# Kernel tuning notes

Hardware: AMD Instinct MI355X
Metric: run time of the kernel (lower is better)

The kernel has to match this reference:

```python
import jax, jax.numpy as jnp
import numpy as np

TOD, DOW = 288, 7
INPUT_LEN, OUTPUT_LEN = 12, 12
N_NODES, R_PATCH, LAYERS = 883, 8, 3
D_IN, D_NODE, D_TOD, D_DOW = 64, 32, 32, 32
DIMS = D_IN + D_NODE + D_TOD + D_DOW  # 160
HID = 2 * DIMS
NEG = -1e9  # finite large-negative mask (avoids NaN on fully-masked rows)


def setup_inputs():
    key = jax.random.key(0)
    ks = jax.random.split(key, 16)
    B = 8
    x = jax.random.normal(ks[0], (B, INPUT_LEN, N_NODES, 1), jnp.float32)
    te = jax.random.randint(ks[1], (B, INPUT_LEN, N_NODES, 2), 0, 7, dtype=jnp.int32)
    s = 0.1
    return {
        "x": x,
        "te": te,
        "patch_emb": jax.random.normal(ks[2], (R_PATCH, D_NODE), jnp.float32) * s,
        "node_table": jax.random.normal(ks[3], (N_NODES, D_NODE), jnp.float32) * s,
        "tod_emb": jax.random.normal(ks[4], (TOD, D_TOD), jnp.float32) * s,
        "dow_emb": jax.random.normal(ks[5], (DOW, D_DOW), jnp.float32) * s,
        "conv_W": jax.random.normal(ks[6], (D_IN, 3, INPUT_LEN), jnp.float32) * s,
        "conv_b": jnp.zeros((D_IN,), jnp.float32),
        # 4 layernorms per layer: [iro1, iro2, ier1, ier2]
        "ln_scale": jnp.ones((LAYERS, 4, DIMS), jnp.float32),
        "ln_bias": jnp.zeros((LAYERS, 4, DIMS), jnp.float32),
        # attn: axis1 = [iro, ier]; axis2 = [q, k, v, out], weights stored [in, out]
        "attn_W": jax.random.normal(ks[7], (LAYERS, 2, 4, DIMS, DIMS), jnp.float32) * 0.05,
        "attn_b": jnp.zeros((LAYERS, 2, 4, DIMS), jnp.float32),
        "mlp_W1": jax.random.normal(ks[8], (LAYERS, 2, DIMS, HID), jnp.float32) * 0.05,
        "mlp_b1": jnp.zeros((LAYERS, 2, HID), jnp.float32),
        "mlp_W2": jax.random.normal(ks[9], (LAYERS, 2, HID, DIMS), jnp.float32) * 0.05,
        "mlp_b2": jnp.zeros((LAYERS, 2, DIMS), jnp.float32),
        "out_W": jax.random.normal(ks[10], (OUTPUT_LEN, DIMS), jnp.float32) * 0.05,
        "out_b": jnp.zeros((OUTPUT_LEN,), jnp.float32),
    }


def _layernorm(x, g, b):
    mu = jnp.mean(x, axis=-1, keepdims=True)
    var = jnp.mean(jnp.square(x - mu), axis=-1, keepdims=True)
    return (x - mu) / jnp.sqrt(var + 1e-5) * g + b


def _mha(x, W, b, key_mask):
    # single-head attention (num_heads=1 in PatchID); x: [..., S, D]
    q = x @ W[0] + b[0]
    k = x @ W[1] + b[1]
    v = x @ W[2] + b[2]
    score = jnp.einsum('...sd,...td->...st', q, k) / np.sqrt(x.shape[-1]).astype(np.float32)
    score = jnp.where(key_mask[..., None, :], score, NEG)
    w = jax.nn.softmax(score, axis=-1)
    o = jnp.einsum('...st,...td->...sd', w, v)
    return o @ W[3] + b[3]


def _forward(x, te, patch_emb, node_table, tod_emb, dow_emb, conv_W, conv_b,
             ln_scale, ln_bias, attn_W, attn_b, mlp_W1, mlp_b1, mlp_W2, mlp_b2,
             out_W, out_b):
    N, R = N_NODES, R_PATCH
    # ---- PatchClassifier (router) ----
    logits = node_table @ patch_emb.T                       # [N, R]
    probs = jax.nn.softmax(logits, axis=-1)
    patch_ids = jnp.argmax(probs, axis=-1)                  # [N]
    hard = jax.nn.one_hot(patch_ids, R, dtype=probs.dtype)
    probs_st = hard - jax.lax.stop_gradient(probs) + probs  # straight-through
    node_soft = probs @ patch_emb                           # [N, D_NODE]
    # ---- embedding ----
    B, T_in = x.shape[0], x.shape[1]
    T = T_in // INPUT_LEN  # = 1
    tef = te.astype(x.dtype)
    x1 = jnp.concatenate([x, tef[..., 0:1] / TOD, tef[..., 1:2] / DOW], axis=-1)  # [B,T_in,N,3]
    x1 = x1.reshape(B, T, INPUT_LEN, N, 3)
    feat = jnp.einsum('btlnc,dcl->btnd', x1, conv_W) + conv_b  # patchified conv
    tid = te[:, -T:, :, 0]
    diw = te[:, -T:, :, 1]
    emb = jnp.concatenate([
        feat, tod_emb[tid], dow_emb[diw],
        jnp.broadcast_to(node_soft, (B, T, N, D_NODE)),
    ], axis=-1)                                             # [B,T,N,DIMS]
    # ---- group_by_patch (static P = N upper bound, masked) ----
    onehot = patch_ids[:, None] == jnp.arange(R)[None, :]
    pos = jnp.cumsum(onehot.astype(jnp.int32), axis=0)[jnp.arange(N), patch_ids] - 1
    P = N
    pf = jnp.zeros((B, T, R, P, DIMS), emb.dtype).at[:, :, patch_ids, pos, :].set(emb)
    mask2d = jnp.zeros((R, P), bool).at[patch_ids, pos].set(True)
    km_iro = mask2d[None, None]       # [1,1,R,P] valid-key mask, keys = P axis
    km_ier = mask2d.T[None, None]     # [1,1,P,R] valid-key mask, keys = R axis
    # ---- encoder layers ----
    for l in range(LAYERS):
        # intra-patch attention over P
        xn = _layernorm(pf, ln_scale[l, 0], ln_bias[l, 0])
        pf = pf + _mha(xn, attn_W[l, 0], attn_b[l, 0], km_iro)
        h = _layernorm(pf, ln_scale[l, 1], ln_bias[l, 1])
        pf = pf + (jax.nn.gelu(h @ mlp_W1[l, 0] + mlp_b1[l, 0], approximate=False)
                   @ mlp_W2[l, 0] + mlp_b2[l, 0])
        # inter-patch attention over R
        xt = jnp.swapaxes(pf, 2, 3)  # [B,T,P,R,D]
        xn = _layernorm(xt, ln_scale[l, 2], ln_bias[l, 2])
        xt = xt + _mha(xn, attn_W[l, 1], attn_b[l, 1], km_ier)
        pf = jnp.swapaxes(xt, 2, 3)
        h = _layernorm(pf, ln_scale[l, 3], ln_bias[l, 3])
        pf = pf + (jax.nn.gelu(h @ mlp_W1[l, 1] + mlp_b1[l, 1], approximate=False)
                   @ mlp_W2[l, 1] + mlp_b2[l, 1])
    # ---- ungroup + 1x1 output conv ----
    out_feat = pf[:, :, patch_ids, pos, :]                  # [B,T,N,DIMS]
    pred = jnp.einsum('btnd,od->bont', out_feat, out_W) + out_b[None, :, None, None]
    return pred, probs_st


def reference(x, te, patch_emb, node_table, tod_emb, dow_emb, conv_W, conv_b,
              ln_scale, ln_bias, attn_W, attn_b, mlp_W1, mlp_b1, mlp_W2, mlp_b2,
              out_W, out_b):
    return _forward(x, te, patch_emb, node_table, tod_emb, dow_emb, conv_W, conv_b,
                    ln_scale, ln_bias, attn_W, attn_b, mlp_W1, mlp_b1, mlp_W2,
                    mlp_b2, out_W, out_b)
```

## Files before the change

### kernel.cpp

```cpp
#include <hip/hip_runtime.h>
#include <hip/hip_cooperative_groups.h>
#include <math.h>

namespace cg = cooperative_groups;

#define NNODES 883
#define BB 8
#define DIMS_ 160
#define HID_ 320
#define PBB 1008
#define RMAX2 (BB*PBB)
#define RMAXP (RMAX2+64)
#define GXNUM (RMAX2/16)

typedef __attribute__((ext_vector_type(8))) short short8v;
typedef __attribute__((ext_vector_type(4))) float fx4;
typedef __attribute__((ext_vector_type(4))) unsigned short ushort4v;

__device__ __forceinline__ unsigned short f2bf(float f) {
  unsigned int u = __float_as_uint(f);
  u = (u + 0x7fffu + ((u >> 16) & 1u)) >> 16;
  return (unsigned short)u;
}
__device__ __forceinline__ float bf2f(unsigned short u) {
  return __uint_as_float(((unsigned int)u) << 16);
}
__device__ __forceinline__ float gelu_f(float v) {
  return 0.5f*v*(1.f + erff(v*0.70710678118654752f));
}

__global__ __launch_bounds__(256)
void zero_pf(float4* __restrict__ p, int n4) {
  int i = blockIdx.x*256 + threadIdx.x;
  if (i < n4) p[i] = float4{0.f, 0.f, 0.f, 0.f};
}

__global__ __launch_bounds__(1024)
void patch_scan(const float* __restrict__ node_table,
                const float* __restrict__ patch_emb,
                float* __restrict__ probs_st,
                float* __restrict__ nsoft,
                int* __restrict__ pk, int* __restrict__ cnt,
                int* __restrict__ offs) {
  __shared__ float pe[256];
  __shared__ int pid_s[NNODES];
  __shared__ int cnt_s[8], offs_s[8];
  int t = threadIdx.x;
  for (int k = t; k < 256; k += 1024) pe[k] = patch_emb[k];
  if (t < 8) cnt_s[t] = 0;
  __syncthreads();
  int am = -1;
  if (t < NNODES) {
    float nt[32];
#pragma unroll
    for (int j = 0; j < 32; ++j) nt[j] = node_table[t*32 + j];
    float lg[8];
#pragma unroll
    for (int r = 0; r < 8; ++r) {
      float a = 0.f;
#pragma unroll
      for (int j = 0; j < 32; ++j) a += nt[j] * pe[r*32 + j];
      lg[r] = a;
    }
    float m = lg[0];
#pragma unroll
    for (int r = 1; r < 8; ++r) m = fmaxf(m, lg[r]);
    float e[8]; float s = 0.f;
#pragma unroll
    for (int r = 0; r < 8; ++r) { e[r] = expf(lg[r] - m); s += e[r]; }
    float p[8];
#pragma unroll
    for (int r = 0; r < 8; ++r) p[r] = e[r] / s;
    am = 0; float best = p[0];
#pragma unroll
    for (int r = 1; r < 8; ++r) if (p[r] > best) { best = p[r]; am = r; }
    pid_s[t] = am;
    atomicAdd(&cnt_s[am], 1);
#pragma unroll
    for (int r = 0; r < 8; ++r) {
      float hard = (r == am) ? 1.f : 0.f;
      probs_st[t*8 + r] = (hard - p[r]) + p[r];
    }
#pragma unroll
    for (int j = 0; j < 32; ++j) {
      float a = 0.f;
#pragma unroll
      for (int r = 0; r < 8; ++r) a += p[r] * pe[r*32 + j];
      nsoft[t*32 + j] = a;
    }
  }
  __syncthreads();
  if (t == 0) {
    int o = 0;
#pragma unroll
    for (int r = 0; r < 8; ++r) {
      offs_s[r] = o; offs[r] = o; cnt[r] = cnt_s[r];
      o += (cnt_s[r] + 15) & ~15;
    }
  }
  __syncthreads();
  if (t < NNODES) {
    int pos = 0;
    for (int m = 0; m < t; ++m) pos += (pid_s[m] == am) ? 1 : 0;
    pk[t] = offs_s[am] + pos;
  }
}

__global__ __launch_bounds__(160)
void embed_kernel(const float* __restrict__ x, const int* __restrict__ te,
                  const float* __restrict__ convW, const float* __restrict__ convB,
                  const float* __restrict__ tod, const float* __restrict__ dow,
                  const float* __restrict__ nsoft, const int* __restrict__ pk,
                  const float* __restrict__ g, const float* __restrict__ bt,
                  float* __restrict__ pf, unsigned short* __restrict__ xn) {
  int n = blockIdx.x, b = blockIdx.y, t = threadIdx.x;
  __shared__ float xs[3][12];
  __shared__ float rsum[160], rss[160];
  __shared__ float musv[2];
  if (t < 12) {
    int l = t;
    xs[0][l] = x[(b*12 + l)*NNODES + n];
    int base = ((b*12 + l)*NNODES + n)*2;
    xs[1][l] = (float)te[base]     / 288.0f;
    xs[2][l] = (float)te[base + 1] / 7.0f;
  }
  __syncthreads();
  int row = b*PBB + pk[n];
  float val;
  if (t < 64) {
    float a = convB[t];
#pragma unroll
    for (int c = 0; c < 3; ++c)
#pragma unroll
      for (int l = 0; l < 12; ++l)
        a += xs[c][l] * convW[t*36 + c*12 + l];
    val = a;
  } else if (t < 96) {
    int ti = te[((b*12 + 11)*NNODES + n)*2 + 0];
    val = tod[ti*32 + (t - 64)];
  } else if (t < 128) {
    int dw = te[((b*12 + 11)*NNODES + n)*2 + 1];
    val = dow[dw*32 + (t - 96)];
  } else {
    val = nsoft[n*32 + (t - 128)];
  }
  pf[row*DIMS_ + t] = val;
  rsum[t] = val; rss[t] = val*val;
  __syncthreads();
  if (t < 32) {
    float s = 0.f, ss = 0.f;
#pragma unroll
    for (int j = 0; j < 5; ++j) { s += rsum[t + 32*j]; ss += rss[t + 32*j]; }
    s  += __shfl_xor(s, 1, 32);  ss += __shfl_xor(ss, 1, 32);
    s  += __shfl_xor(s, 2, 32);  ss += __shfl_xor(ss, 2, 32);
    s  += __shfl_xor(s, 4, 32);  ss += __shfl_xor(ss, 4, 32);
    s  += __shfl_xor(s, 8, 32);  ss += __shfl_xor(ss, 8, 32);
    s  += __shfl_xor(s, 16, 32); ss += __shfl_xor(ss, 16, 32);
    if (t == 0) {
      float mu = s*(1.f/160.f);
      float var = ss*(1.f/160.f) - mu*mu;
      musv[0] = mu; musv[1] = rsqrtf(var + 1e-5f);
    }
  }
  __syncthreads();
  xn[(size_t)row*DIMS_ + t] = f2bf((val - musv[0])*musv[1]*g[t] + bt[t]);
}

__global__ __launch_bounds__(256)
void cvt_all(const float* __restrict__ attn_W, const float* __restrict__ mlp_W1,
             const float* __restrict__ mlp_W2,
             unsigned short* __restrict__ wt_attn, unsigned short* __restrict__ wt_w1,
             unsigned short* __restrict__ wt_w2) {
  int y = blockIdx.y;
  const float* src; unsigned short* dst; int K, N;
  if (y < 24)      { src = attn_W + (size_t)y*25600;        dst = wt_attn + (size_t)y*25600; K = 160; N = 160; }
  else if (y < 30) { int q = y-24; src = mlp_W1 + (size_t)q*160*320; dst = wt_w1 + (size_t)q*51200; K = 160; N = 320; }
  else             { int q = y-30; src = mlp_W2 + (size_t)q*320*160; dst = wt_w2 + (size_t)q*51200; K = 320; N = 160; }
  int tn = N >> 5, tk = K >> 5;
  int tile = blockIdx.x;
  if (tile >= tn*tk) return;
  int n0 = (tile % tn) << 5, k0 = (tile / tn) << 5;
  __shared__ unsigned short lds[32][33];
  int col = threadIdx.x & 31, rb = threadIdx.x >> 5;
#pragma unroll
  for (int rr = 0; rr < 4; ++rr) {
    int row = rb + 8*rr;
    lds[row][col] = f2bf(src[(size_t)(k0 + row)*N + n0 + col]);
  }
  __syncthreads();
#pragma unroll
  for (int rr = 0; rr < 4; ++rr) {
    int row = rb + 8*rr;
    dst[(size_t)(n0 + row)*K + k0 + col] = lds[col][row];
  }
}

__device__ __forceinline__ void qkv_from_L1(const char* L1,
    const unsigned short* __restrict__ wq, const float* __restrict__ bq,
    unsigned short* __restrict__ qbN, bool transv,
    int row0, int wid, int r15, int kg) {
  constexpr size_t CY = (size_t)(RMAX2 + 16) * DIMS_;
  fx4 accq[4];
#pragma unroll
  for (int u = 0; u < 4; ++u) accq[u] = (fx4){0.f,0.f,0.f,0.f};
#pragma unroll
  for (int t = 0; t < 5; ++t) {
    short8v a4 = *(const short8v*)(const void*)(L1 + r15*384 + ((t*64 + kg*16) ^ ((r15 & 7) << 4)));
#pragma unroll
    for (int u = 0; u < 4; ++u) {
      int n = wid + 8*u;
      if (n < 30) {
        int z = n / 10, nn = n - z*10;
        short8v bfr = *(const short8v*)(const void*)
            (wq + (size_t)z*25600 + (size_t)(nn*16 + r15)*160 + t*32 + kg*8);
        accq[u] = __builtin_amdgcn_mfma_f32_16x16x32_bf16(a4, bfr, accq[u], 0, 0, 0);
      }
    }
  }
#pragma unroll
  for (int u = 0; u < 4; ++u) {
    int n = wid + 8*u;
    if (n >= 30) continue;
    int z = n / 10, nn = n - z*10;
    int col = nn*16 + r15;
    float bv = bq[z*160 + col];
    unsigned short* C = qbN + (size_t)z * CY;
#pragma unroll
    for (int i = 0; i < 4; ++i) {
      int rr = row0 + 4*kg + i;
      unsigned short h = f2bf(accq[u][i] + bv);
      if (transv && z == 2) C[(size_t)col*RMAXP + rr] = h;
      else                  C[(size_t)rr*DIMS_ + col] = h;
    }
  }
}

__global__ __launch_bounds__(512, 4)
void layers_coop(unsigned short* __restrict__ qbA, unsigned short* __restrict__ qbB,
                 const unsigned short* __restrict__ wt_attn,
                 const unsigned short* __restrict__ wt_w1,
                 const unsigned short* __restrict__ wt_w2,
                 const float* __restrict__ attn_b, const float* __restrict__ mlp_b1,
                 const float* __restrict__ mlp_b2,
                 const float* __restrict__ ln_scale, const float* __restrict__ ln_bias,
                 const unsigned short* __restrict__ xn, float* __restrict__ pf,
                 const int* __restrict__ cnt, const int* __restrict__ offs) {
  constexpr size_t CY = (size_t)(RMAX2 + 16) * DIMS_;
  cg::grid_group gg = cg::this_grid();
  __shared__ unsigned short L1s[16*192];
  __shared__ unsigned short L2s[16*320];
  __shared__ float sA[8][16], ssA[8][16];
  __shared__ float Sf[16*256];
  __shared__ unsigned short Pl[16*256];
  __shared__ float Sinv[16];
  __shared__ int cs[8], os[8];
  char* L1 = (char*)L1s; char* L2 = (char*)L2s; char* Pb = (char*)Pl;
  const float scale = 0.07905694150420949f;

  int tid = threadIdx.x;
  int wid = tid >> 6;
  int lane = tid & 63;
  int r15 = lane & 15, kg = lane >> 4;
  int row0 = blockIdx.x * 16;
  if (tid < 8) { cs[tid] = cnt[tid]; os[tid] = offs[tid]; }
  __syncthreads();
  int b = row0 / PBB;
  int local = row0 - b*PBB;
  int r = 7;
#pragma unroll
  for (int rr = 6; rr >= 0; --rr) if (local < os[rr+1]) r = rr;
  int L = cs[r];
  int q0 = local - os[r];
  int bo = b*PBB + os[r];
  int ntP = (wid < 2) ? 2 : 1;
  int ntM = (wid < 4) ? 3 : 2;

  float trunk[2][4];
#pragma unroll
  for (int u = 0; u < 2; ++u)
    if (u < ntP) {
      int col = (wid + 8*u)*16 + r15;
#pragma unroll
      for (int i = 0; i < 4; ++i)
        trunk[u][i] = pf[(size_t)(row0 + 4*kg + i)*DIMS_ + col];
    }

  for (int k = tid; k < 16*DIMS_; k += 512) {
    int row = k / DIMS_, col = k - row*DIMS_;
    int byte = row*384 + ((col*2) ^ ((row & 7) << 4));
    *(unsigned short*)(L1 + byte) = xn[(size_t)(row0 + row)*DIMS_ + col];
  }
  __syncthreads();
  qkv_from_L1(L1, wt_attn, attn_b, qbA, true, row0, wid, r15, kg);
  __threadfence();
  gg.sync();

  for (int wb = 0; wb < 6; ++wb) {
    bool intra = ((wb & 1) == 0);
    bool hasnext = (wb < 5);
    unsigned short* qbCur = (wb & 1) ? qbB : qbA;
    unsigned short* qbNext = (wb & 1) ? qbA : qbB;
    const unsigned short* qb = qbCur;
    const unsigned short* kb = qbCur + CY;
    const unsigned short* vt = qbCur + 2*CY;
    const unsigned short* wqkv = wt_attn + (size_t)wb*4*25600;
    const float* bbase = attn_b + (size_t)wb*4*DIMS_;
    const unsigned short* wproj = wqkv + 3*25600;
    const float* bproj = bbase + 3*DIMS_;
    const unsigned short* w1 = wt_w1 + (size_t)wb*51200;
    const unsigned short* w2 = wt_w2 + (size_t)wb*51200;
    const float* b1v = mlp_b1 + (size_t)wb*HID_;
    const float* b2v = mlp_b2 + (size_t)wb*DIMS_;
    const float* g1  = ln_scale + (size_t)(2*wb + 1)*DIMS_;
    const float* bt1 = ln_bias  + (size_t)(2*wb + 1)*DIMS_;
    const float* gn  = ln_scale + (size_t)(2*wb + 2)*DIMS_;
    const float* btn = ln_bias  + (size_t)(2*wb + 2)*DIMS_;
    const unsigned short* wqkvN = wt_attn + (size_t)(wb+1)*4*25600;
    const float* bqkvN = attn_b + (size_t)(wb+1)*4*DIMS_;

    if (intra) {
      int nkt = (L + 15) >> 4;
      int npv = (L + 31) >> 5;
      short8v qf[5];
      {
        const unsigned short* Qr = qb + (size_t)(row0 + r15)*DIMS_ + kg*8;
#pragma unroll
        for (int kk = 0; kk < 5; ++kk) qf[kk] = *(const short8v*)(const void*)(Qr + kk*32);
      }
#pragma unroll
      for (int u = 0; u < 2; ++u) {
        int t = wid + 8*u;
        if (t < nkt) {
          fx4 a = (fx4){0.f,0.f,0.f,0.f};
          const unsigned short* Kr = kb + (size_t)(bo + t*16 + r15)*DIMS_ + kg*8;
#pragma unroll
          for (int kk = 0; kk < 5; ++kk) {
            short8v kf = *(const short8v*)(const void*)(Kr + kk*32);
            a = __builtin_amdgcn_mfma_f32_16x16x32_bf16(qf[kk], kf, a, 0, 0, 0);
          }
          int j = t*16 + r15;
#pragma unroll
          for (int i = 0; i < 4; ++i)
            Sf[(4*kg + i)*256 + j] = (j < L) ? a[i]*scale : -1e30f;
        }
      }
      __syncthreads();
      {
        int qq = lane >> 5, l32 = lane & 31;
        int row = 2*wid + qq;
        float vals[8];
        float mx = -1e30f;
#pragma unroll
        for (int k = 0; k < 8; ++k) {
          int j = l32 + 32*k;
          float v = (j < L) ? Sf[row*256 + j] : -1e30f;
          vals[k] = v; mx = fmaxf(mx, v);
        }
        mx = fmaxf(mx, __shfl_xor(mx, 1, 32));
        mx = fmaxf(mx, __shfl_xor(mx, 2, 32));
        mx = fmaxf(mx, __shfl_xor(mx, 4, 32));
        mx = fmaxf(mx, __shfl_xor(mx, 8, 32));
        mx = fmaxf(mx, __shfl_xor(mx, 16, 32));
        float sum = 0.f;
#pragma unroll
        for (int k = 0; k < 8; ++k) {
          float e = (vals[k] > -1e29f) ? expf(vals[k] - mx) : 0.f;
          vals[k] = e; sum += e;
        }
        sum += __shfl_xor(sum, 1, 32);
        sum += __shfl_xor(sum, 2, 32);
        sum += __shfl_xor(sum, 4, 32);
        sum += __shfl_xor(sum, 8, 32);
        sum += __shfl_xor(sum, 16, 32);
        if (l32 == 0) Sinv[row] = (sum > 0.f) ? 1.f/sum : 0.f;
#pragma unroll
        for (int k = 0; k < 8; ++k) {
          int j = l32 + 32*k;
          int byte = row*512 + ((j*2) ^ ((row & 7) << 4));
          *(unsigned short*)(Pb + byte) = f2bf(vals[k]);
        }
      }
      __syncthreads();
      fx4 o[2];
#pragma unroll
      for (int u = 0; u < 2; ++u) o[u] = (fx4){0.f,0.f,0.f,0.f};
#pragma unroll
      for (int sS = 0; sS < 8; ++sS) {
        if (sS < npv) {
          short8v pfr = *(const short8v*)(const void*)
              (Pb + r15*512 + ((sS*64 + kg*16) ^ ((r15 & 7) << 4)));
#pragma unroll
          for (int u = 0; u < 2; ++u)
            if (u < ntP) {
              int n = wid + 8*u;
              const unsigned short* Vr = vt + (size_t)(n*16 + r15)*RMAXP + bo + sS*32 + kg*8;
              short8v vf = *(const short8v*)(const void*)Vr;
              o[u] = __builtin_amdgcn_mfma_f32_16x16x32_bf16(pfr, vf, o[u], 0, 0, 0);
            }
        }
      }
      float inv[4];
#pragma unroll
      for (int i = 0; i < 4; ++i) inv[i] = Sinv[4*kg + i];
#pragma unroll
      for (int u = 0; u < 2; ++u)
        if (u < ntP) {
          int n = wid + 8*u;
#pragma unroll
          for (int i = 0; i < 4; ++i) {
            int row = 4*kg + i, d = n*16 + r15;
            int byte = row*384 + ((d*2) ^ ((row & 7) << 4));
            *(unsigned short*)(L1 + byte) = f2bf(o[u][i]*inv[i]);
          }
        }
    } else {
      int qq = lane >> 5, l32 = lane & 31;
      int rowT = 2*wid + qq;
      int p = q0 + rowT;
      bool vq = p < L;
      int j = l32 >> 2, c = l32 & 3;
      int cj = cs[j];
      bool vk = p < cj;
      int keyrow = b*PBB + os[j] + (vk ? p : 0);
      int qrow = row0 + rowT;
      float part = 0.f;
      {
        const unsigned short* qr = qb + (size_t)qrow*DIMS_ + c*40;
        const unsigned short* kr = kb + (size_t)keyrow*DIMS_ + c*40;
#pragma unroll
        for (int dd = 0; dd < 5; ++dd) {
          short8v a8 = *(const short8v*)(const void*)(qr + dd*8);
          short8v b8 = *(const short8v*)(const void*)(kr + dd*8);
#pragma unroll
          for (int u = 0; u < 8; ++u)
            part += bf2f((unsigned short)a8[u]) * bf2f((unsigned short)b8[u]);
        }
      }
      part += __shfl_xor(part, 1, 4);
      part += __shfl_xor(part, 2, 4);
      float sc = (vq && vk) ? part*scale : -1e30f;
      float m = sc;
      m = fmaxf(m, __shfl_xor(m, 4, 32));
      m = fmaxf(m, __shfl_xor(m, 8, 32));
      m = fmaxf(m, __shfl_xor(m, 16, 32));
      float e = (vq && vk) ? expf(sc - m) : 0.f;
      float sum = e;
      sum += __shfl_xor(sum, 4, 32);
      sum += __shfl_xor(sum, 8, 32);
      sum += __shfl_xor(sum, 16, 32);
      float w = (vq && vk && sum > 0.f) ? e/sum : 0.f;
      float o[5];
#pragma unroll
      for (int k = 0; k < 5; ++k) o[k] = 0.f;
      int qbase = qq*32;
#pragma unroll
      for (int jj = 0; jj < 8; ++jj) {
        float wv = __shfl(w, qbase + jj*4);
        int kr2 = __shfl(keyrow, qbase + jj*4);
        if (wv > 0.f) {
          const unsigned short* Vr = vt + (size_t)kr2*DIMS_;
#pragma unroll
          for (int k = 0; k < 5; ++k) o[k] += wv * bf2f(Vr[l32 + 32*k]);
        }
      }
#pragma unroll
      for (int k = 0; k < 5; ++k) {
        int d = l32 + 32*k;
        int byte = rowT*384 + ((d*2) ^ ((rowT & 7) << 4));
        *(unsigned short*)(L1 + byte) = f2bf(vq ? o[k] : 0.f);
      }
    }
    __syncthreads();

    short8v af[5];
#pragma unroll
    for (int t = 0; t < 5; ++t)
      af[t] = *(const short8v*)(const void*)(L1 + r15*384 + ((t*64 + kg*16) ^ ((r15 & 7) << 4)));
    fx4 acc[2];
#pragma unroll
    for (int u = 0; u < 2; ++u) acc[u] = (fx4){0.f,0.f,0.f,0.f};
#pragma unroll
    for (int t = 0; t < 5; ++t)
#pragma unroll
      for (int u = 0; u < 2; ++u)
        if (u < ntP) {
          int n = wid + 8*u;
          short8v bfr = *(const short8v*)(const void*)(wproj + (size_t)(n*16 + r15)*160 + t*32 + kg*8);
          acc[u] = __builtin_amdgcn_mfma_f32_16x16x32_bf16(af[t], bfr, acc[u], 0, 0, 0);
        }

    float sv[4] = {0,0,0,0}, ssv[4] = {0,0,0,0};
#pragma unroll
    for (int u = 0; u < 2; ++u)
      if (u < ntP) {
        int n = wid + 8*u;
        int col = n*16 + r15;
        float bv = bproj[col];
#pragma unroll
        for (int i = 0; i < 4; ++i) {
          float v = trunk[u][i] + acc[u][i] + bv;
          trunk[u][i] = v;
          sv[i] += v; ssv[i] += v*v;
        }
      }
#pragma unroll
    for (int i = 0; i < 4; ++i) {
      sv[i] += __shfl_xor(sv[i], 1, 16); ssv[i] += __shfl_xor(ssv[i], 1, 16);
      sv[i] += __shfl_xor(sv[i], 2, 16); ssv[i] += __shfl_xor(ssv[i], 2, 16);
      sv[i] += __shfl_xor(sv[i], 4, 16); ssv[i] += __shfl_xor(ssv[i], 4, 16);
      sv[i] += __shfl_xor(sv[i], 8, 16); ssv[i] += __shfl_xor(ssv[i], 8, 16);
    }
    if (r15 == 0) {
#pragma unroll
      for (int i = 0; i < 4; ++i) { sA[wid][4*kg+i] = sv[i]; ssA[wid][4*kg+i] = ssv[i]; }
    }
    __syncthreads();
    float mu[4], rs[4];
#pragma unroll
    for (int i = 0; i < 4; ++i) {
      float st = 0.f, sst = 0.f;
#pragma unroll
      for (int w = 0; w < 8; ++w) { st += sA[w][4*kg+i]; sst += ssA[w][4*kg+i]; }
      mu[i] = st*(1.f/160.f);
      float var = sst*(1.f/160.f) - mu[i]*mu[i];
      rs[i] = rsqrtf(var + 1e-5f);
    }
#pragma unroll
    for (int u = 0; u < 2; ++u)
      if (u < ntP) {
        int n = wid + 8*u;
        int col = n*16 + r15;
        float gv = g1[col], bv = bt1[col];
#pragma unroll
        for (int i = 0; i < 4; ++i) {
          int row = 4*kg + i;
          int byte = row*384 + ((col*2) ^ ((row & 7) << 4));
          *(unsigned short*)(L1 + byte) = f2bf((trunk[u][i] - mu[i])*rs[i]*gv + bv);
        }
      }
    __syncthreads();

    fx4 acc2[3];
#pragma unroll
    for (int u = 0; u < 3; ++u) acc2[u] = (fx4){0.f,0.f,0.f,0.f};
#pragma unroll
    for (int t = 0; t < 5; ++t) {
      short8v a2 = *(const short8v*)(const void*)(L1 + r15*384 + ((t*64 + kg*16) ^ ((r15 & 7) << 4)));
#pragma unroll
      for (int u = 0; u < 3; ++u)
        if (u < ntM) {
          int n = wid + 8*u;
          short8v bfr = *(const short8v*)(const void*)(w1 + (size_t)(n*16 + r15)*160 + t*32 + kg*8);
          acc2[u] = __builtin_amdgcn_mfma_f32_16x16x32_bf16(a2, bfr, acc2[u], 0, 0, 0);
        }
    }
#pragma unroll
    for (int u = 0; u < 3; ++u)
      if (u < ntM) {
        int n = wid + 8*u;
        int col = n*16 + r15;
        float bv = b1v[col];
#pragma unroll
        for (int i = 0; i < 4; ++i) {
          float v = gelu_f(acc2[u][i] + bv);
          int row = 4*kg + i;
          int byte = row*640 + ((col*2) ^ ((row & 7) << 4));
          *(unsigned short*)(L2 + byte) = f2bf(v);
        }
      }
    __syncthreads();

    fx4 acc3[2];
#pragma unroll
    for (int u = 0; u < 2; ++u) acc3[u] = (fx4){0.f,0.f,0.f,0.f};
#pragma unroll
    for (int t = 0; t < 10; ++t) {
      short8v a3 = *(const short8v*)(const void*)(L2 + r15*640 + ((t*64 + kg*16) ^ ((r15 & 7) << 4)));
#pragma unroll
      for (int u = 0; u < 2; ++u)
        if (u < ntP) {
          int n = wid + 8*u;
          short8v bfr = *(const short8v*)(const void*)(w2 + (size_t)(n*16 + r15)*320 + t*32 + kg*8);
          acc3[u] = __builtin_amdgcn_mfma_f32_16x16x32_bf16(a3, bfr, acc3[u], 0, 0, 0);
        }
    }
    float sv2[4] = {0,0,0,0}, ssv2[4] = {0,0,0,0};
#pragma unroll
    for (int u = 0; u < 2; ++u)
      if (u < ntP) {
        int n = wid + 8*u;
        int col = n*16 + r15;
        float bv = b2v[col];
#pragma unroll
        for (int i = 0; i < 4; ++i) {
          float v = trunk[u][i] + acc3[u][i] + bv;
          trunk[u][i] = v;
          sv2[i] += v; ssv2[i] += v*v;
        }
      }

    if (hasnext) {
#pragma unroll
      for (int i = 0; i < 4; ++i) {
        sv2[i] += __shfl_xor(sv2[i], 1, 16); ssv2[i] += __shfl_xor(ssv2[i], 1, 16);
        sv2[i] += __shfl_xor(sv2[i], 2, 16); ssv2[i] += __shfl_xor(ssv2[i], 2, 16);
        sv2[i] += __shfl_xor(sv2[i], 4, 16); ssv2[i] += __shfl_xor(ssv2[i], 4, 16);
        sv2[i] += __shfl_xor(sv2[i], 8, 16); ssv2[i] += __shfl_xor(ssv2[i], 8, 16);
      }
      __syncthreads();
      if (r15 == 0) {
#pragma unroll
        for (int i = 0; i < 4; ++i) { sA[wid][4*kg+i] = sv2[i]; ssA[wid][4*kg+i] = ssv2[i]; }
      }
      __syncthreads();
#pragma unroll
      for (int i = 0; i < 4; ++i) {
        float st = 0.f, sst = 0.f;
#pragma unroll
        for (int w = 0; w < 8; ++w) { st += sA[w][4*kg+i]; sst += ssA[w][4*kg+i]; }
        mu[i] = st*(1.f/160.f);
        float var = sst*(1.f/160.f) - mu[i]*mu[i];
        rs[i] = rsqrtf(var + 1e-5f);
      }
#pragma unroll
      for (int u = 0; u < 2; ++u)
        if (u < ntP) {
          int n = wid + 8*u;
          int col = n*16 + r15;
          float gv = gn[col], bv = btn[col];
#pragma unroll
          for (int i = 0; i < 4; ++i) {
            int row = 4*kg + i;
            int byte = row*384 + ((col*2) ^ ((row & 7) << 4));
            *(unsigned short*)(L1 + byte) = f2bf((trunk[u][i] - mu[i])*rs[i]*gv + bv);
          }
        }
      __syncthreads();

      qkv_from_L1(L1, wqkvN, bqkvN, qbNext, (wb & 1) != 0, row0, wid, r15, kg);
      __threadfence();
      gg.sync();
    }
  }

#pragma unroll
  for (int u = 0; u < 2; ++u)
    if (u < ntP) {
      int col = (wid + 8*u)*16 + r15;
#pragma unroll
      for (int i = 0; i < 4; ++i)
        pf[(size_t)(row0 + 4*kg + i)*DIMS_ + col] = trunk[u][i];
    }
}

template<bool INTRA, bool HASNEXT, bool TRANSV_NEXT>
__global__ __launch_bounds__(512)
void fused_layer(const unsigned short* __restrict__ qb,
                 const unsigned short* __restrict__ kb,
                 const unsigned short* __restrict__ vt,
                 const unsigned short* __restrict__ wproj, const float* __restrict__ bproj,
                 const unsigned short* __restrict__ w1, const float* __restrict__ b1v,
                 const unsigned short* __restrict__ w2, const float* __restrict__ b2v,
                 const float* __restrict__ g1, const float* __restrict__ bt1,
                 const float* __restrict__ gn, const float* __restrict__ btn,
                 const unsigned short* __restrict__ wqkvN, const float* __restrict__ bqkvN,
                 float* __restrict__ pf, unsigned short* __restrict__ qbN,
                 const int* __restrict__ cnt, const int* __restrict__ offs) {
  __shared__ unsigned short L1s[16*192];
  __shared__ unsigned short L2s[16*320];
  __shared__ float sA[8][16], ssA[8][16];
  __shared__ float Sf[INTRA ? 16*256 : 1];
  __shared__ unsigned short Pl[INTRA ? 16*256 : 1];
  __shared__ float Sinv[16];
  __shared__ int cs[8], os[8];
  char* L1 = (char*)L1s; char* L2 = (char*)L2s; char* Pb = (char*)Pl;
  const float scale = 0.07905694150420949f;

  int tid = threadIdx.x;
  int wid = tid >> 6;
  int lane = tid & 63;
  int r15 = lane & 15, kg = lane >> 4;
  int row0 = blockIdx.x * 16;
  if (tid < 8) { cs[tid] = cnt[tid]; os[tid] = offs[tid]; }
  __syncthreads();
  int b = row0 / PBB;
  int local = row0 - b*PBB;
  int r = 7;
#pragma unroll
  for (int rr = 6; rr >= 0; --rr) if (local < os[rr+1]) r = rr;
  int L = cs[r];
  int q0 = local - os[r];
  int bo = b*PBB + os[r];
  int ntP = (wid < 2) ? 2 : 1;
  int ntM = (wid < 4) ? 3 : 2;

  if (INTRA) {
    int nkt = (L + 15) >> 4;
    int npv = (L + 31) >> 5;
    short8v qf[5];
    {
      const unsigned short* Qr = qb + (size_t)(row0 + r15)*DIMS_ + kg*8;
#pragma unroll
      for (int kk = 0; kk < 5; ++kk) qf[kk] = *(const short8v*)(const void*)(Qr + kk*32);
    }
#pragma unroll
    for (int u = 0; u < 2; ++u) {
      int t = wid + 8*u;
      if (t < nkt) {
        fx4 a = (fx4){0.f,0.f,0.f,0.f};
        const unsigned short* Kr = kb + (size_t)(bo + t*16 + r15)*DIMS_ + kg*8;
#pragma unroll
        for (int kk = 0; kk < 5; ++kk) {
          short8v kf = *(const short8v*)(const void*)(Kr + kk*32);
          a = __builtin_amdgcn_mfma_f32_16x16x32_bf16(qf[kk], kf, a, 0, 0, 0);
        }
        int j = t*16 + r15;
#pragma unroll
        for (int i = 0; i < 4; ++i)
          Sf[(4*kg + i)*256 + j] = (j < L) ? a[i]*scale : -1e30f;
      }
    }
    __syncthreads();
    {
      int qq = lane >> 5, l32 = lane & 31;
      int row = 2*wid + qq;
      float vals[8];
      float mx = -1e30f;
#pragma unroll
      for (int k = 0; k < 8; ++k) {
        int j = l32 + 32*k;
        float v = (j < L) ? Sf[row*256 + j] : -1e30f;
        vals[k] = v; mx = fmaxf(mx, v);
      }
      mx = fmaxf(mx, __shfl_xor(mx, 1, 32));
      mx = fmaxf(mx, __shfl_xor(mx, 2, 32));
      mx = fmaxf(mx, __shfl_xor(mx, 4, 32));
      mx = fmaxf(mx, __shfl_xor(mx, 8, 32));
      mx = fmaxf(mx, __shfl_xor(mx, 16, 32));
      float sum = 0.f;
#pragma unroll
      for (int k = 0; k < 8; ++k) {
        float e = (vals[k] > -1e29f) ? expf(vals[k] - mx) : 0.f;
        vals[k] = e; sum += e;
      }
      sum += __shfl_xor(sum, 1, 32);
      sum += __shfl_xor(sum, 2, 32);
      sum += __shfl_xor(sum, 4, 32);
      sum += __shfl_xor(sum, 8, 32);
      sum += __shfl_xor(sum, 16, 32);
      if (l32 == 0) Sinv[row] = (sum > 0.f) ? 1.f/sum : 0.f;
#pragma unroll
      for (int k = 0; k < 8; ++k) {
        int j = l32 + 32*k;
        int byte = row*512 + ((j*2) ^ ((row & 7) << 4));
        *(unsigned short*)(Pb + byte) = f2bf(vals[k]);
      }
    }
    __syncthreads();
    fx4 o[2];
#pragma unroll
    for (int u = 0; u < 2; ++u) o[u] = (fx4){0.f,0.f,0.f,0.f};
#pragma unroll
    for (int sS = 0; sS < 8; ++sS) {
      if (sS < npv) {
        short8v pfr = *(const short8v*)(const void*)
            (Pb + r15*512 + ((sS*64 + kg*16) ^ ((r15 & 7) << 4)));
#pragma unroll
        for (int u = 0; u < 2; ++u)
          if (u < ntP) {
            int n = wid + 8*u;
            const unsigned short* Vr = vt + (size_t)(n*16 + r15)*RMAXP + bo + sS*32 + kg*8;
            short8v vf = *(const short8v*)(const void*)Vr;
            o[u] = __builtin_amdgcn_mfma_f32_16x16x32_bf16(pfr, vf, o[u], 0, 0, 0);
          }
      }
    }
    float inv[4];
#pragma unroll
    for (int i = 0; i < 4; ++i) inv[i] = Sinv[4*kg + i];
#pragma unroll
    for (int u = 0; u < 2; ++u)
      if (u < ntP) {
        int n = wid + 8*u;
#pragma unroll
        for (int i = 0; i < 4; ++i) {
          int row = 4*kg + i, d = n*16 + r15;
          int byte = row*384 + ((d*2) ^ ((row & 7) << 4));
          *(unsigned short*)(L1 + byte) = f2bf(o[u][i]*inv[i]);
        }
      }
  } else {
    int qq = lane >> 5, l32 = lane & 31;
    int rowT = 2*wid + qq;
    int p = q0 + rowT;
    bool vq = p < L;
    int j = l32 >> 2, c = l32 & 3;
    int cj = cs[j];
    bool vk = p < cj;
    int keyrow = b*PBB + os[j] + (vk ? p : 0);
    int qrow = row0 + rowT;
    float part = 0.f;
    {
      const unsigned short* qr = qb + (size_t)qrow*DIMS_ + c*40;
      const unsigned short* kr = kb + (size_t)keyrow*DIMS_ + c*40;
#pragma unroll
      for (int dd = 0; dd < 5; ++dd) {
        short8v a8 = *(const short8v*)(const void*)(qr + dd*8);
        short8v b8 = *(const short8v*)(const void*)(kr + dd*8);
#pragma unroll
        for (int u = 0; u < 8; ++u)
          part += bf2f((unsigned short)a8[u]) * bf2f((unsigned short)b8[u]);
      }
    }
    part += __shfl_xor(part, 1, 4);
    part += __shfl_xor(part, 2, 4);
    float sc = (vq && vk) ? part*scale : -1e30f;
    float m = sc;
    m = fmaxf(m, __shfl_xor(m, 4, 32));
    m = fmaxf(m, __shfl_xor(m, 8, 32));
    m = fmaxf(m, __shfl_xor(m, 16, 32));
    float e = (vq && vk) ? expf(sc - m) : 0.f;
    float sum = e;
    sum += __shfl_xor(sum, 4, 32);
    sum += __shfl_xor(sum, 8, 32);
    sum += __shfl_xor(sum, 16, 32);
    float w = (vq && vk && sum > 0.f) ? e/sum : 0.f;
    float o[5];
#pragma unroll
    for (int k = 0; k < 5; ++k) o[k] = 0.f;
    int qbase = qq*32;
#pragma unroll
    for (int jj = 0; jj < 8; ++jj) {
      float wv = __shfl(w, qbase + jj*4);
      int kr2 = __shfl(keyrow, qbase + jj*4);
      if (wv > 0.f) {
        const unsigned short* Vr = vt + (size_t)kr2*DIMS_;
#pragma unroll
        for (int k = 0; k < 5; ++k) o[k] += wv * bf2f(Vr[l32 + 32*k]);
      }
    }
#pragma unroll
    for (int k = 0; k < 5; ++k) {
      int d = l32 + 32*k;
      int byte = rowT*384 + ((d*2) ^ ((rowT & 7) << 4));
      *(unsigned short*)(L1 + byte) = f2bf(vq ? o[k] : 0.f);
    }
  }
  __syncthreads();

  short8v af[5];
#pragma unroll
  for (int t = 0; t < 5; ++t)
    af[t] = *(const short8v*)(const void*)(L1 + r15*384 + ((t*64 + kg*16) ^ ((r15 & 7) << 4)));
  fx4 acc[2];
#pragma unroll
  for (int u = 0; u < 2; ++u) acc[u] = (fx4){0.f,0.f,0.f,0.f};
#pragma unroll
  for (int t = 0; t < 5; ++t)
#pragma unroll
    for (int u = 0; u < 2; ++u)
      if (u < ntP) {
        int n = wid + 8*u;
        short8v bfr = *(const short8v*)(const void*)(wproj + (size_t)(n*16 + r15)*160 + t*32 + kg*8);
        acc[u] = __builtin_amdgcn_mfma_f32_16x16x32_bf16(af[t], bfr, acc[u], 0, 0, 0);
      }

  float pn[2][4];
  float sv[4] = {0,0,0,0}, ssv[4] = {0,0,0,0};
#pragma unroll
  for (int u = 0; u < 2; ++u)
    if (u < ntP) {
      int n = wid + 8*u;
      int col = n*16 + r15;
      float bv = bproj[col];
#pragma unroll
      for (int i = 0; i < 4; ++i) {
        int row = row0 + 4*kg + i;
        float v = pf[(size_t)row*DIMS_ + col] + acc[u][i] + bv;
        pn[u][i] = v;
        pf[(size_t)row*DIMS_ + col] = v;
        sv[i] += v; ssv[i] += v*v;
      }
    }
#pragma unroll
  for (int i = 0; i < 4; ++i) {
    sv[i] += __shfl_xor(sv[i], 1, 16); ssv[i] += __shfl_xor(ssv[i], 1, 16);
    sv[i] += __shfl_xor(sv[i], 2, 16); ssv[i] += __shfl_xor(ssv[i], 2, 16);
    sv[i] += __shfl_xor(sv[i], 4, 16); ssv[i] += __shfl_xor(ssv[i], 4, 16);
    sv[i] += __shfl_xor(sv[i], 8, 16); ssv[i] += __shfl_xor(ssv[i], 8, 16);
  }
  if (r15 == 0) {
#pragma unroll
    for (int i = 0; i < 4; ++i) { sA[wid][4*kg+i] = sv[i]; ssA[wid][4*kg+i] = ssv[i]; }
  }
  __syncthreads();
  float mu[4], rs[4];
#pragma unroll
  for (int i = 0; i < 4; ++i) {
    float st = 0.f, sst = 0.f;
#pragma unroll
    for (int w = 0; w < 8; ++w) { st += sA[w][4*kg+i]; sst += ssA[w][4*kg+i]; }
    mu[i] = st*(1.f/160.f);
    float var = sst*(1.f/160.f) - mu[i]*mu[i];
    rs[i] = rsqrtf(var + 1e-5f);
  }
#pragma unroll
  for (int u = 0; u < 2; ++u)
    if (u < ntP) {
      int n = wid + 8*u;
      int col = n*16 + r15;
      float gv = g1[col], bv = bt1[col];
#pragma unroll
      for (int i = 0; i < 4; ++i) {
        int row = 4*kg + i;
        int byte = row*384 + ((col*2) ^ ((row & 7) << 4));
        *(unsigned short*)(L1 + byte) = f2bf((pn[u][i] - mu[i])*rs[i]*gv + bv);
      }
    }
  __syncthreads();

  fx4 acc2[3];
#pragma unroll
  for (int u = 0; u < 3; ++u) acc2[u] = (fx4){0.f,0.f,0.f,0.f};
#pragma unroll
  for (int t = 0; t < 5; ++t) {
    short8v a2 = *(const short8v*)(const void*)(L1 + r15*384 + ((t*64 + kg*16) ^ ((r15 & 7) << 4)));
#pragma unroll
    for (int u = 0; u < 3; ++u)
      if (u < ntM) {
        int n = wid + 8*u;
        short8v bfr = *(const short8v*)(const void*)(w1 + (size_t)(n*16 + r15)*160 + t*32 + kg*8);
        acc2[u] = __builtin_amdgcn_mfma_f32_16x16x32_bf16(a2, bfr, acc2[u], 0, 0, 0);
      }
  }
#pragma unroll
  for (int u = 0; u < 3; ++u)
    if (u < ntM) {
      int n = wid + 8*u;
      int col = n*16 + r15;
      float bv = b1v[col];
#pragma unroll
      for (int i = 0; i < 4; ++i) {
        float v = gelu_f(acc2[u][i] + bv);
        int row = 4*kg + i;
        int byte = row*640 + ((col*2) ^ ((row & 7) << 4));
        *(unsigned short*)(L2 + byte) = f2bf(v);
      }
    }
  __syncthreads();

  fx4 acc3[2];
#pragma unroll
  for (int u = 0; u < 2; ++u) acc3[u] = (fx4){0.f,0.f,0.f,0.f};
#pragma unroll
  for (int t = 0; t < 10; ++t) {
    short8v a3 = *(const short8v*)(const void*)(L2 + r15*640 + ((t*64 + kg*16) ^ ((r15 & 7) << 4)));
#pragma unroll
    for (int u = 0; u < 2; ++u)
      if (u < ntP) {
        int n = wid + 8*u;
        short8v bfr = *(const short8v*)(const void*)(w2 + (size_t)(n*16 + r15)*320 + t*32 + kg*8);
        acc3[u] = __builtin_amdgcn_mfma_f32_16x16x32_bf16(a3, bfr, acc3[u], 0, 0, 0);
      }
  }
  float sv2[4] = {0,0,0,0}, ssv2[4] = {0,0,0,0};
  float fnv[2][4];
#pragma unroll
  for (int u = 0; u < 2; ++u)
    if (u < ntP) {
      int n = wid + 8*u;
      int col = n*16 + r15;
      float bv = b2v[col];
#pragma unroll
      for (int i = 0; i < 4; ++i) {
        float v = pn[u][i] + acc3[u][i] + bv;
        fnv[u][i] = v;
        pf[(size_t)(row0 + 4*kg + i)*DIMS_ + col] = v;
        sv2[i] += v; ssv2[i] += v*v;
      }
    }
  if (!HASNEXT) return;

#pragma unroll
  for (int i = 0; i < 4; ++i) {
    sv2[i] += __shfl_xor(sv2[i], 1, 16); ssv2[i] += __shfl_xor(ssv2[i], 1, 16);
    sv2[i] += __shfl_xor(sv2[i], 2, 16); ssv2[i] += __shfl_xor(ssv2[i], 2, 16);
    sv2[i] += __shfl_xor(sv2[i], 4, 16); ssv2[i] += __shfl_xor(ssv2[i], 4, 16);
    sv2[i] += __shfl_xor(sv2[i], 8, 16); ssv2[i] += __shfl_xor(ssv2[i], 8, 16);
  }
  __syncthreads();
  if (r15 == 0) {
#pragma unroll
    for (int i = 0; i < 4; ++i) { sA[wid][4*kg+i] = sv2[i]; ssA[wid][4*kg+i] = ssv2[i]; }
  }
  __syncthreads();
#pragma unroll
  for (int i = 0; i < 4; ++i) {
    float st = 0.f, sst = 0.f;
#pragma unroll
    for (int w = 0; w < 8; ++w) { st += sA[w][4*kg+i]; sst += ssA[w][4*kg+i]; }
    mu[i] = st*(1.f/160.f);
    float var = sst*(1.f/160.f) - mu[i]*mu[i];
    rs[i] = rsqrtf(var + 1e-5f);
  }
#pragma unroll
  for (int u = 0; u < 2; ++u)
    if (u < ntP) {
      int n = wid + 8*u;
      int col = n*16 + r15;
      float gv = gn[col], bv = btn[col];
#pragma unroll
      for (int i = 0; i < 4; ++i) {
        int row = 4*kg + i;
        int byte = row*384 + ((col*2) ^ ((row & 7) << 4));
        *(unsigned short*)(L1 + byte) = f2bf((fnv[u][i] - mu[i])*rs[i]*gv + bv);
      }
    }
  __syncthreads();

  qkv_from_L1(L1, wqkvN, bqkvN, qbN, TRANSV_NEXT, row0, wid, r15, kg);
}

__global__ __launch_bounds__(512)
void qkv0_kernel(const unsigned short* __restrict__ xn,
                 const unsigned short* __restrict__ wt_attn, const float* __restrict__ attn_b,
                 unsigned short* __restrict__ qbA) {
  __shared__ unsigned short L1s[16*192];
  char* L1 = (char*)L1s;
  int tid = threadIdx.x;
  int wid = tid >> 6, lane = tid & 63;
  int r15 = lane & 15, kg = lane >> 4;
  int row0 = blockIdx.x * 16;
  for (int k = tid; k < 16*DIMS_; k += 512) {
    int row = k / DIMS_, col = k - row*DIMS_;
    int byte = row*384 + ((col*2) ^ ((row & 7) << 4));
    *(unsigned short*)(L1 + byte) = xn[(size_t)(row0 + row)*DIMS_ + col];
  }
  __syncthreads();
  qkv_from_L1(L1, wt_attn, attn_b, qbA, true, row0, wid, r15, kg);
}

__global__ __launch_bounds__(256)
void out_kernel(const float* __restrict__ pf, const float* __restrict__ outW,
                const float* __restrict__ outB, const int* __restrict__ pk,
                float* __restrict__ out) {
  int idx = blockIdx.x*256 + threadIdx.x;
  if (idx >= BB*12*NNODES) return;
  int n = idx % NNODES;
  int rest = idx / NNODES;
  int o = rest % 12;
  int b = rest / 12;
  int row = b*PBB + pk[n];
  const float4* Pr = (const float4*)&pf[(size_t)row*DIMS_];
  const float4* Wr = (const float4*)&outW[o*DIMS_];
  float ax=0.f, ay=0.f, az=0.f, aw=0.f;
#pragma unroll
  for (int d4 = 0; d4 < 40; ++d4) {
    float4 a = Pr[d4], c = Wr[d4];
    ax += a.x*c.x; ay += a.y*c.y; az += a.z*c.z; aw += a.w*c.w;
  }
  out[idx] = (ax+ay+az+aw) + outB[o];
}

extern "C" void kernel_launch(void* const* d_in, const int* in_sizes, int n_in,
                              void* d_out, int out_size, void* d_ws, size_t ws_size,
                              hipStream_t stream) {
  const float* x         = (const float*)d_in[0];
  const int*   te        = (const int*)d_in[1];
  const float* patch_emb = (const float*)d_in[2];
  const float* node_tab  = (const float*)d_in[3];
  const float* tod_emb   = (const float*)d_in[4];
  const float* dow_emb   = (const float*)d_in[5];
  const float* conv_W    = (const float*)d_in[6];
  const float* conv_b    = (const float*)d_in[7];
  const float* ln_scale  = (const float*)d_in[8];
  const float* ln_bias   = (const float*)d_in[9];
  const float* attn_W    = (const float*)d_in[10];
  const float* attn_b    = (const float*)d_in[11];
  const float* mlp_W1    = (const float*)d_in[12];
  const float* mlp_b1    = (const float*)d_in[13];
  const float* mlp_W2    = (const float*)d_in[14];
  const float* mlp_b2    = (const float*)d_in[15];
  const float* out_W     = (const float*)d_in[16];
  const float* out_b     = (const float*)d_in[17];

  float* out = (float*)d_out;
  float* probs_st = out + BB*12*NNODES;

  const size_t CY = (size_t)(RMAX2 + 16) * DIMS_;
  const size_t QBSZ = 2*CY + (size_t)DIMS_*RMAXP;

  char* W = (char*)d_ws;
  float* pf = (float*)W;                        W += (size_t)(RMAX2 + 16)*DIMS_*4;
  unsigned short* xn = (unsigned short*)W;      W += (size_t)(RMAX2 + 16)*DIMS_*2;
  unsigned short* qbA = (unsigned short*)W;     W += QBSZ*2;
  unsigned short* qbB = (unsigned short*)W;     W += QBSZ*2;
  unsigned short* wt_attn = (unsigned short*)W; W += (size_t)24*160*160*2;
  unsigned short* wt_w1   = (unsigned short*)W; W += (size_t)6*320*160*2;
  unsigned short* wt_w2   = (unsigned short*)W; W += (size_t)6*160*320*2;
  float* nsoft = (float*)W;                     W += (size_t)NNODES*32*4;
  int* pk   = (int*)W;
  int* cnt  = pk + NNODES;
  int* offs = cnt + 8;

  {
    int n4 = (RMAX2 + 16) * DIMS_ / 4;
    zero_pf<<<(n4 + 255)/256, 256, 0, stream>>>((float4*)pf, n4);
  }
  cvt_all<<<dim3(50, 36), 256, 0, stream>>>(attn_W, mlp_W1, mlp_W2, wt_attn, wt_w1, wt_w2);
  patch_scan<<<1, 1024, 0, stream>>>(node_tab, patch_emb, probs_st, nsoft, pk, cnt, offs);
  embed_kernel<<<dim3(NNODES, BB), 160, 0, stream>>>(x, te, conv_W, conv_b, tod_emb, dow_emb,
                                                     nsoft, pk, ln_scale, ln_bias, pf, xn);

  int maxb = 0;
  hipError_t occ = hipOccupancyMaxActiveBlocksPerMultiprocessor(&maxb, (const void*)layers_coop, 512, 0);
  bool coop_ok = (occ == hipSuccess) && (maxb * 256 >= GXNUM);

  if (coop_ok) {
    void* args[] = {(void*)&qbA, (void*)&qbB, (void*)&wt_attn, (void*)&wt_w1, (void*)&wt_w2,
                    (void*)&attn_b, (void*)&mlp_b1, (void*)&mlp_b2,
                    (void*)&ln_scale, (void*)&ln_bias, (void*)&xn, (void*)&pf,
                    (void*)&cnt, (void*)&offs};
    hipError_t e = hipLaunchCooperativeKernel((const void*)layers_coop,
                                              dim3(GXNUM), dim3(512), args, 0, stream);
    coop_ok = (e == hipSuccess);
  }

  if (!coop_ok) {
    qkv0_kernel<<<GXNUM, 512, 0, stream>>>(xn, wt_attn, attn_b, qbA);
    for (int wb = 0; wb < 6; ++wb) {
      unsigned short* qbCur = (wb & 1) ? qbB : qbA;
      unsigned short* qbNext = (wb & 1) ? qbA : qbB;
      const unsigned short* wqkv = wt_attn + (size_t)wb*4*25600;
      const float* bbase = attn_b + (size_t)wb*4*DIMS_;
      const unsigned short* wproj = wqkv + 3*25600;
      const float* bproj = bbase + 3*DIMS_;
      const unsigned short* w1 = wt_w1 + (size_t)wb*51200;
      const unsigned short* w2 = wt_w2 + (size_t)wb*51200;
      const float* b1v = mlp_b1 + (size_t)wb*HID_;
      const float* b2v = mlp_b2 + (size_t)wb*DIMS_;
      const float* g1  = ln_scale + (size_t)(2*wb + 1)*DIMS_;
      const float* bt1 = ln_bias  + (size_t)(2*wb + 1)*DIMS_;
      const float* gn  = ln_scale + (size_t)(2*wb + 2)*DIMS_;
      const float* btn = ln_bias  + (size_t)(2*wb + 2)*DIMS_;
      const unsigned short* wqkvN = wt_attn + (size_t)(wb+1)*4*25600;
      const float* bqkvN = attn_b + (size_t)(wb+1)*4*DIMS_;
      if (wb == 5)
        fused_layer<false,false,false><<<GXNUM, 512, 0, stream>>>(
            qbCur, qbCur + CY, qbCur + 2*CY, wproj, bproj, w1, b1v, w2, b2v,
            g1, bt1, nullptr, nullptr, nullptr, nullptr, pf, qbNext, cnt, offs);
      else if ((wb & 1) == 0)
        fused_layer<true,true,false><<<GXNUM, 512, 0, stream>>>(
            qbCur, qbCur + CY, qbCur + 2*CY, wproj, bproj, w1, b1v, w2, b2v,
            g1, bt1, gn, btn, wqkvN, bqkvN, pf, qbNext, cnt, offs);
      else
        fused_layer<false,true,true><<<GXNUM, 512, 0, stream>>>(
            qbCur, qbCur + CY, qbCur + 2*CY, wproj, bproj, w1, b1v, w2, b2v,
            g1, bt1, gn, btn, wqkvN, bqkvN, pf, qbNext, cnt, offs);
    }
  }

  out_kernel<<<(BB*12*NNODES + 255)/256, 256, 0, stream>>>(pf, out_W, out_b, pk, out);
}
```

Measured before the change: 261.4 us.

## Replace grid-wide barriers with per-block dependency flags in cooperative layer kernel

Each block now publishes a release flag per layer stage once its QKV output is written, and before each attention stage waits only on the specific producer blocks it reads from (the key tiles of its patch for intra, or the blocks covering its rows across patches for inter). This replaces the full grid.sync between stages, so fast blocks can run ahead instead of waiting on the slowest block in the grid. It adds a flag buffer, a kernel to zero it, and spin-wait loops with relaxed loads followed by a threadfence. Correctness depends on the dependency sets being complete and on the memory ordering being sufficient, and there is a risk of reading stale data or write-after-read hazards on the double-buffered qb arrays that the old barrier guarded against.

```diff
diff --git a/kernel.cpp b/kernel.cpp
--- a/kernel.cpp
+++ b/kernel.cpp
@@ -1,8 +1,6 @@
 #include <hip/hip_runtime.h>
 #include <hip/hip_cooperative_groups.h>
 #include <math.h>
-
-namespace cg = cooperative_groups;
 
 #define NNODES 883
 #define BB 8
@@ -33,6 +31,12 @@
 void zero_pf(float4* __restrict__ p, int n4) {
   int i = blockIdx.x*256 + threadIdx.x;
   if (i < n4) p[i] = float4{0.f, 0.f, 0.f, 0.f};
+}
+
+__global__ __launch_bounds__(256)
+void zero_flags(int* __restrict__ f, int n) {
+  int i = blockIdx.x*256 + threadIdx.x;
+  if (i < n) f[i] = 0;
 }
 
 __global__ __launch_bounds__(1024)
@@ -244,9 +248,9 @@
                  const float* __restrict__ mlp_b2,
                  const float* __restrict__ ln_scale, const float* __restrict__ ln_bias,
                  const unsigned short* __restrict__ xn, float* __restrict__ pf,
-                 const int* __restrict__ cnt, const int* __restrict__ offs) {
+                 const int* __restrict__ cnt, const int* __restrict__ offs,
+                 int* __restrict__ flags) {
   constexpr size_t CY = (size_t)(RMAX2 + 16) * DIMS_;
-  cg::grid_group gg = cg::this_grid();
   __shared__ unsigned short L1s[16*192];
   __shared__ unsigned short L2s[16*320];
   __shared__ float sA[8][16], ssA[8][16];
@@ -293,7 +297,9 @@
   __syncthreads();
   qkv_from_L1(L1, wt_attn, attn_b, qbA, true, row0, wid, r15, kg);
   __threadfence();
-  gg.sync();
+  __syncthreads();
+  if (tid == 0)
+    __hip_atomic_store(&flags[0*GXNUM + (int)blockIdx.x], 1, __ATOMIC_RELEASE, __HIP_MEMORY_SCOPE_AGENT);
 
   for (int wb = 0; wb < 6; ++wb) {
     bool intra = ((wb & 1) == 0);
@@ -318,6 +324,24 @@
     const unsigned short* wqkvN = wt_attn + (size_t)(wb+1)*4*25600;
     const float* bqkvN = attn_b + (size_t)(wb+1)*4*DIMS_;
 
+    {
+      const int fbase = wb*GXNUM;
+      if (intra) {
+        int nkt = (L + 15) >> 4;
+        int blk0 = bo >> 4;
+        if (tid < nkt) {
+          while (__hip_atomic_load(&flags[fbase + blk0 + tid], __ATOMIC_RELAXED, __HIP_MEMORY_SCOPE_AGENT) == 0) {}
+        }
+      } else {
+        if (tid < 8 && q0 < cs[tid]) {
+          int dep = (b*PBB + os[tid] + q0) >> 4;
+          while (__hip_atomic_load(&flags[fbase + dep], __ATOMIC_RELAXED, __HIP_MEMORY_SCOPE_AGENT) == 0) {}
+        }
+      }
+      __syncthreads();
+      __threadfence();
+    }
+
     if (intra) {
       int nkt = (L + 15) >> 4;
       int npv = (L + 31) >> 5;
@@ -639,7 +663,9 @@
 
       qkv_from_L1(L1, wqkvN, bqkvN, qbNext, (wb & 1) != 0, row0, wid, r15, kg);
       __threadfence();
-      gg.sync();
+      __syncthreads();
+      if (tid == 0)
+        __hip_atomic_store(&flags[(wb+1)*GXNUM + (int)blockIdx.x], 1, __ATOMIC_RELEASE, __HIP_MEMORY_SCOPE_AGENT);
     }
   }
 
@@ -1099,6 +1125,7 @@
   unsigned short* wt_w1   = (unsigned short*)W; W += (size_t)6*320*160*2;
   unsigned short* wt_w2   = (unsigned short*)W; W += (size_t)6*160*320*2;
   float* nsoft = (float*)W;                     W += (size_t)NNODES*32*4;
+  int* flags = (int*)W;                         W += (size_t)6*GXNUM*4;
   int* pk   = (int*)W;
   int* cnt  = pk + NNODES;
   int* offs = cnt + 8;
@@ -1107,6 +1134,7 @@
     int n4 = (RMAX2 + 16) * DIMS_ / 4;
     zero_pf<<<(n4 + 255)/256, 256, 0, stream>>>((float4*)pf, n4);
   }
+  zero_flags<<<(6*GXNUM + 255)/256, 256, 0, stream>>>(flags, 6*GXNUM);
   cvt_all<<<dim3(50, 36), 256, 0, stream>>>(attn_W, mlp_W1, mlp_W2, wt_attn, wt_w1, wt_w2);
   patch_scan<<<1, 1024, 0, stream>>>(node_tab, patch_emb, probs_st, nsoft, pk, cnt, offs);
   embed_kernel<<<dim3(NNODES, BB), 160, 0, stream>>>(x, te, conv_W, conv_b, tod_emb, dow_emb,
@@ -1120,7 +1148,7 @@
     void* args[] = {(void*)&qbA, (void*)&qbB, (void*)&wt_attn, (void*)&wt_w1, (void*)&wt_w2,
                     (void*)&attn_b, (void*)&mlp_b1, (void*)&mlp_b2,
                     (void*)&ln_scale, (void*)&ln_bias, (void*)&xn, (void*)&pf,
-                    (void*)&cnt, (void*)&offs};
+                    (void*)&cnt, (void*)&offs, (void*)&flags};
     hipError_t e = hipLaunchCooperativeKernel((const void*)layers_coop,
                                               dim3(GXNUM), dim3(512), args, 0, stream);
     coop_ok = (e == hipSuccess);
```

New measurement: 263.4 us, median of 2. Within noise of the previous version (+0.8%).
